# Kernel tuning notes

Hardware: AMD Instinct MI355X
Metric: run time of the kernel (lower is better)

Reference implementation:

```python
import jax, jax.numpy as jnp
import numpy as np

B, N, K, DIMS, F_DIMS = 2, 32768, 16, 2, 32
DS, DH, DO = 32, 32, 32
DA = DS + DH                      # 64
CH = (DIMS + 1) * (1 + K) + DIMS  # 53
CONV_IN = DIMS + (1 + K) * DA     # 1090
CONV_OUT = (1 + K) * DO           # 544


def setup_inputs() -> dict:
    key = jax.random.key(0)
    ks = jax.random.split(key, 6)
    s = 0.05
    return {
        "pc": jax.random.normal(ks[0], (B, N, 1 + K, DIMS), jnp.float32),
        "feats": jax.random.normal(ks[1], (B, N, 1 + K, F_DIMS), jnp.float32),
        "W_mlp": jax.random.normal(ks[2], (CH, DS), jnp.float32) * s,
        "b_mlp": jnp.zeros((DS,), jnp.float32),
        "W_att": jax.random.normal(ks[3], (DA, DA), jnp.float32) * s,
        "b_att": jnp.zeros((DA,), jnp.float32),
        "W_conv": jax.random.normal(ks[4], (CONV_IN, CONV_OUT), jnp.float32) * s,
        "b_conv": jnp.zeros((CONV_OUT,), jnp.float32),
        "W_skip": jax.random.normal(ks[5], (DO + F_DIMS, DO), jnp.float32) * s,
        "b_skip": jnp.zeros((DO,), jnp.float32),
    }


def reference(pc, feats, W_mlp, b_mlp, W_att, b_att, W_conv, b_conv, W_skip, b_skip):
    # ---- LocSE: relative-position encoding ----
    # rpbn_i[b,n,j] = concat(pc[b,n,i] - pc[b,n,j], ||pc[b,n,j]||)
    norms = jnp.linalg.norm(pc, axis=-1, keepdims=True)          # (B,N,1+K,1)
    # diffs[b,n,j,i,:] = pc[b,n,i,:] - pc[b,n,j,:]
    diffs = pc[:, :, None, :, :] - pc[:, :, :, None, :]          # (B,N,1+K,1+K,dims)
    norms_b = jnp.broadcast_to(norms[:, :, :, None, :], diffs.shape[:-1] + (1,))
    blocks = jnp.concatenate([diffs, norms_b], axis=-1)          # (B,N,1+K,1+K,dims+1)
    blocks = blocks.reshape(pc.shape[:3] + ((1 + K) * (DIMS + 1),))
    rppe = jnp.concatenate([pc, blocks], axis=-1)                # (B,N,1+K,CH)
    r = jax.nn.relu(rppe @ W_mlp + b_mlp)                        # (B,N,1+K,DS)
    se = jnp.concatenate([r, feats], axis=-1)                    # (B,N,1+K,DA)

    # ---- attention pooling (softmax over channel axis) ----
    att = jax.nn.softmax(se @ W_att + b_att, axis=-1) * se       # (B,N,1+K,DA)
    reshaped = att.reshape(att.shape[0], att.shape[1], (1 + K) * DA)

    cat = jnp.concatenate([pc[:, :, 0], reshaped], axis=-1)      # (B,N,CONV_IN)
    res = jax.nn.relu(cat @ W_conv + b_conv)                     # (B,N,(1+K)*DO)
    res = res.reshape(res.shape[0], res.shape[1], 1 + K, DO)

    skip_in = jnp.concatenate([feats, res], axis=-1)             # (B,N,1+K,F+DO)
    skip = jax.nn.relu(skip_in @ W_skip + b_skip)                # (B,N,1+K,DO)
    return skip
```

## Files before the change

### kernel.cpp

```cpp
#include <hip/hip_runtime.h>
#include <hip/hip_bf16.h>
#include <cstdint>

#define KNB      17
#define CH       53
#define MP       16
#define BM       64
#define NTHR     512
#define NRT      17
#define SE_LD    72
#define CATW     1120
#define RES_LD   552

#define NE_CONV  (35*34*512)
#define NE_MLP   (2*2*512)
#define NE_ATT   (2*4*512)
#define NE_SKIP  (2*2*512)
#define WS_MLP   (NE_CONV)
#define WS_ATT   (WS_MLP + NE_MLP)
#define WS_SKIP  (WS_ATT + NE_ATT)
#define WS_TOTAL (WS_SKIP + NE_SKIP)

typedef __bf16 bf16x8 __attribute__((ext_vector_type(8)));
typedef float  f32x4  __attribute__((ext_vector_type(4)));
typedef unsigned short u16x4 __attribute__((ext_vector_type(4)));
typedef unsigned short u16x8 __attribute__((ext_vector_type(8)));

__device__ __forceinline__ unsigned short f2b(float f) {
    union { __bf16 h; unsigned short u; } v; v.h = (__bf16)f; return v.u;
}
__device__ __forceinline__ float b2f(unsigned short b) {
    union { unsigned u; float f; } v; v.u = ((unsigned)b) << 16;
    return v.f;
}
__device__ __forceinline__ void gload_lds16(const void* g, void* l) {
    __builtin_amdgcn_global_load_lds(
        (const __attribute__((address_space(1))) unsigned int*)g,
        (__attribute__((address_space(3))) unsigned int*)l, 16, 0, 0);
}

__global__ void seac_prep(const float* __restrict__ Wmlp, const float* __restrict__ Watt,
                          const float* __restrict__ Wconv, const float* __restrict__ Wskip,
                          unsigned short* __restrict__ ws)
{
    int i = blockIdx.x * 256 + threadIdx.x;
    if (i >= WS_TOTAL) return;
    float v;
    if (i < WS_MLP) {
        int idx = i;
        int jj = idx & 7, l = (idx >> 3) & 63, t = idx >> 9;
        int nt = t % 34, ks = t / 34;
        int k = 32*ks + 8*(l >> 4) + jj;
        int o = 16*nt + (l & 15);
        int ok;
        if (k < 1088)       ok = k + 2;
        else if (k == 1088) ok = 0;
        else if (k == 1089) ok = 1;
        else                ok = -1;
        v = (ok >= 0) ? Wconv[ok*544 + o] : 0.f;
    } else if (i < WS_ATT) {
        int idx = i - WS_MLP;
        int jj = idx & 7, l = (idx >> 3) & 63, t = idx >> 9;
        int nt = t & 1, ks = t >> 1;
        int k = 32*ks + 8*(l >> 4) + jj;
        int o = 16*nt + (l & 15);
        v = (k < CH) ? Wmlp[k*32 + o] : 0.f;
    } else if (i < WS_SKIP) {
        int idx = i - WS_ATT;
        int jj = idx & 7, l = (idx >> 3) & 63, t = idx >> 9;
        int nt = t & 3, ks = t >> 2;
        int k = 32*ks + 8*(l >> 4) + jj;
        int o = 16*nt + (l & 15);
        v = Watt[k*64 + o];
    } else {
        int idx = i - WS_SKIP;
        int jj = idx & 7, l = (idx >> 3) & 63, t = idx >> 9;
        int nt = t & 1, ks = t >> 1;
        int k = 32*ks + 8*(l >> 4) + jj;
        int o = 16*nt + (l & 15);
        v = Wskip[k*32 + o];
    }
    ws[i] = f2b(v);
}

__global__ __launch_bounds__(NTHR, 6) void seac_locse(
    const float* __restrict__ pc, const float* __restrict__ feats,
    const float* __restrict__ bmlp, const float* __restrict__ batt,
    const unsigned short* __restrict__ ws, unsigned short* __restrict__ catg,
    int pt0)
{
    __shared__ unsigned short se_l[272 * SE_LD];
    __shared__ float pcl[MP][KNB][2];
    __shared__ float bmlp_l[32];
    __shared__ float batt_l[64];

    const int tid  = threadIdx.x;
    const int w    = tid >> 6;
    const int l    = tid & 63;
    const int g    = l >> 4;
    const int c15  = l & 15;
    const long pbase = (long)pt0 + (long)blockIdx.x * MP;
    const bf16x8* wsB8 = (const bf16x8*)ws;

    if (tid < MP*KNB) {
        int p = tid / KNB, i = tid - p*KNB;
        float x = pc[(pbase + p)*(KNB*2) + 2*i];
        float y = pc[(pbase + p)*(KNB*2) + 2*i + 1];
        pcl[p][i][0] = x; pcl[p][i][1] = y;
    }
    for (int q = tid; q < MP*544/4; q += NTHR) {
        float4 f = *(const float4*)&feats[pbase*544 + 4*q];
        int e0 = 4*q; int p = e0 / 544; int rem = e0 - 544*p;
        int j = rem >> 5, c = rem & 31;
        u16x4 u; u[0] = f2b(f.x); u[1] = f2b(f.y); u[2] = f2b(f.z); u[3] = f2b(f.w);
        *(u16x4*)&se_l[(p*KNB + j)*SE_LD + 32 + c] = u;
    }
    if (tid < 32)                     bmlp_l[tid]      = bmlp[tid];
    else if (tid >= 64 && tid < 128)  batt_l[tid-64]   = batt[tid-64];
    __syncthreads();

    {
        bf16x8 Bm[2][2];
        #pragma unroll
        for (int ks = 0; ks < 2; ++ks)
            #pragma unroll
            for (int nt = 0; nt < 2; ++nt)
                Bm[ks][nt] = wsB8[(WS_MLP >> 3) + (ks*2 + nt)*64 + l];
        float bch[2][4];
        #pragma unroll
        for (int nt = 0; nt < 2; ++nt)
            #pragma unroll
            for (int r = 0; r < 4; ++r) bch[nt][r] = bmlp_l[16*nt + 4*g + r];

        for (int mt = w; mt < NRT; mt += 8) {
            int row = 16*mt + c15;
            int p = row / KNB, j = row - p*KNB;
            float pjx = pcl[p][j][0], pjy = pcl[p][j][1];
            float nj = sqrtf(pjx*pjx + pjy*pjy);
            f32x4 acc0 = {0.f,0.f,0.f,0.f}, acc1 = {0.f,0.f,0.f,0.f};
            #pragma unroll
            for (int ks = 0; ks < 2; ++ks) {
                union { unsigned short u[8]; bf16x8 v; } a;
                #pragma unroll
                for (int jj = 0; jj < 8; ++jj) {
                    int k = 32*ks + 8*g + jj;
                    float vv;
                    if (k == 0) vv = pjx;
                    else if (k == 1) vv = pjy;
                    else if (k < CH) {
                        int kk = k - 2, ii = kk/3, t3 = kk - 3*ii;
                        vv = (t3 == 0) ? (pcl[p][ii][0] - pjx)
                           : (t3 == 1) ? (pcl[p][ii][1] - pjy) : nj;
                    } else vv = 0.f;
                    a.u[jj] = f2b(vv);
                }
                acc0 = __builtin_amdgcn_mfma_f32_16x16x32_bf16(Bm[ks][0], a.v, acc0, 0, 0, 0);
                acc1 = __builtin_amdgcn_mfma_f32_16x16x32_bf16(Bm[ks][1], a.v, acc1, 0, 0, 0);
            }
            u16x4 o0, o1;
            #pragma unroll
            for (int r = 0; r < 4; ++r) {
                o0[r] = f2b(fmaxf(acc0[r] + bch[0][r], 0.f));
                o1[r] = f2b(fmaxf(acc1[r] + bch[1][r], 0.f));
            }
            *(u16x4*)&se_l[row*SE_LD + 4*g]      = o0;
            *(u16x4*)&se_l[row*SE_LD + 16 + 4*g] = o1;
        }
    }
    __syncthreads();

    {
        bf16x8 Ba[2][4];
        #pragma unroll
        for (int ks = 0; ks < 2; ++ks)
            #pragma unroll
            for (int nt = 0; nt < 4; ++nt)
                Ba[ks][nt] = wsB8[(WS_ATT >> 3) + (ks*4 + nt)*64 + l];
        float bch[16];
        #pragma unroll
        for (int nt = 0; nt < 4; ++nt)
            #pragma unroll
            for (int r = 0; r < 4; ++r) bch[4*nt+r] = batt_l[16*nt + 4*g + r];

        for (int mt = w; mt < NRT; mt += 8) {
            int row = 16*mt + c15;
            bf16x8 b0 = *(const bf16x8*)&se_l[row*SE_LD + 8*g];
            bf16x8 b1 = *(const bf16x8*)&se_l[row*SE_LD + 32 + 8*g];
            f32x4 acc[4];
            #pragma unroll
            for (int nt = 0; nt < 4; ++nt) {
                f32x4 z = {0.f,0.f,0.f,0.f};
                acc[nt] = __builtin_amdgcn_mfma_f32_16x16x32_bf16(Ba[0][nt], b0, z,       0, 0, 0);
                acc[nt] = __builtin_amdgcn_mfma_f32_16x16x32_bf16(Ba[1][nt], b1, acc[nt], 0, 0, 0);
            }
            float vv[16];
            #pragma unroll
            for (int nt = 0; nt < 4; ++nt)
                #pragma unroll
                for (int r = 0; r < 4; ++r) vv[4*nt+r] = acc[nt][r] + bch[4*nt+r];
            float m = vv[0];
            #pragma unroll
            for (int i = 1; i < 16; ++i) m = fmaxf(m, vv[i]);
            m = fmaxf(m, __shfl_xor(m, 16)); m = fmaxf(m, __shfl_xor(m, 32));
            float s = 0.f;
            #pragma unroll
            for (int i = 0; i < 16; ++i) { vv[i] = __expf(vv[i] - m); s += vv[i]; }
            s += __shfl_xor(s, 16); s += __shfl_xor(s, 32);
            float inv = 1.f / s;
            #pragma unroll
            for (int nt = 0; nt < 4; ++nt) {
                u16x4 sv = *(const u16x4*)&se_l[row*SE_LD + 16*nt + 4*g];
                u16x4 ov;
                #pragma unroll
                for (int r = 0; r < 4; ++r) ov[r] = f2b(vv[4*nt+r]*inv * b2f(sv[r]));
                *(u16x4*)&se_l[row*SE_LD + 16*nt + 4*g] = ov;
            }
        }
    }
    __syncthreads();

    for (int c = tid; c < MP*140; c += NTHR) {
        int p = c / 140, rem = c - 140*p;
        int e = 8*rem;
        u16x8 v;
        if (e < 1088) {
            int row = p*KNB + (e >> 6), col = e & 63;
            v = *(const u16x8*)&se_l[row*SE_LD + col];
        } else {
            #pragma unroll
            for (int q = 0; q < 8; ++q) v[q] = 0;
            if (e == 1088) { v[0] = f2b(pcl[p][0][0]); v[1] = f2b(pcl[p][0][1]); }
        }
        *(u16x8*)&catg[(pbase + p)*CATW + e] = v;
    }
}

__global__ __launch_bounds__(NTHR, 4) void seac_conv(
    const unsigned short* __restrict__ catg, const float* __restrict__ feats,
    const float* __restrict__ bconv, const float* __restrict__ bskip,
    const unsigned short* __restrict__ ws, float* __restrict__ out, int pt0)
{
    __shared__ unsigned short astage[4][BM][32];
    __shared__ unsigned short res_l[32 * RES_LD];
    __shared__ float bconv_l[544];

    const int tid  = threadIdx.x;
    const int w    = tid >> 6;
    const int l    = tid & 63;
    const int g    = l >> 4;
    const int c15  = l & 15;
    const long pbase = (long)pt0 + (long)blockIdx.x * BM;
    const bf16x8* wsB8 = (const bf16x8*)ws;

    for (int i = tid; i < 544; i += NTHR) bconv_l[i] = bconv[i];

    if (tid < 256) {
        const unsigned short* g0 = &catg[(pbase + (tid >> 2))*CATW + 8*(tid & 3)];
        gload_lds16(g0,      &astage[0][16*(tid >> 6)][0]);
        gload_lds16(g0 + 32, &astage[1][16*(tid >> 6)][0]);
        gload_lds16(g0 + 64, &astage[2][16*(tid >> 6)][0]);
    }

    f32x4 acc[4][5];
    #pragma unroll
    for (int mt = 0; mt < 4; ++mt)
        #pragma unroll
        for (int t = 0; t < 5; ++t) { f32x4 z = {0.f,0.f,0.f,0.f}; acc[mt][t] = z; }

    for (int ks = 0; ks < 35; ++ks) {
        asm volatile("s_waitcnt vmcnt(2)" ::: "memory");
        __builtin_amdgcn_s_barrier();
        __builtin_amdgcn_sched_barrier(0);
        bf16x8 a[4];
        #pragma unroll
        for (int mt = 0; mt < 4; ++mt)
            a[mt] = *(const bf16x8*)&astage[ks & 3][16*mt + c15][8*g];
        #pragma unroll
        for (int t = 0; t < 5; ++t) {
            int nt = w + 8*t;
            if (nt < 34) {
                bf16x8 b = wsB8[(ks*34 + nt)*64 + l];
                #pragma unroll
                for (int mt = 0; mt < 4; ++mt)
                    acc[mt][t] = __builtin_amdgcn_mfma_f32_16x16x32_bf16(a[mt], b, acc[mt][t], 0, 0, 0);
            }
        }
        if (ks + 3 < 35 && tid < 256)
            gload_lds16(&catg[(pbase + (tid >> 2))*CATW + 32*(ks+3) + 8*(tid & 3)],
                        &astage[(ks+3) & 3][16*(tid >> 6)][0]);
    }
    __syncthreads();

    bf16x8 Bs[2][2];
    #pragma unroll
    for (int ks = 0; ks < 2; ++ks)
        #pragma unroll
        for (int nt = 0; nt < 2; ++nt)
            Bs[ks][nt] = wsB8[(WS_SKIP >> 3) + (ks*2 + nt)*64 + l];
    float bs0 = bskip[c15], bs1 = bskip[16 + c15];

    #pragma unroll
    for (int half = 0; half < 2; ++half) {
        #pragma unroll
        for (int t = 0; t < 5; ++t) {
            int nt = w + 8*t;
            if (nt < 34) {
                float bc = bconv_l[16*nt + c15];
                #pragma unroll
                for (int mh = 0; mh < 2; ++mh) {
                    int mt = 2*half + mh;
                    #pragma unroll
                    for (int r = 0; r < 4; ++r)
                        res_l[(16*mh + 4*g + r)*RES_LD + 16*nt + c15] =
                            f2b(fmaxf(acc[mt][t][r] + bc, 0.f));
                }
            }
        }
        __syncthreads();

        const long gofs = pbase*KNB + 544*half;
        for (int tt = 0; tt < 5; ++tt) {
            int mt2 = w + 8*tt;
            if (mt2 < 34) {
                int rr = 16*mt2 + c15;
                int pp = rr / 17, jn = rr - 17*pp;
                float4 f0 = *(const float4*)&feats[(gofs + rr)*32 + 8*g];
                float4 f1 = *(const float4*)&feats[(gofs + rr)*32 + 8*g + 4];
                union { unsigned short u[8]; bf16x8 v; } af;
                af.u[0]=f2b(f0.x); af.u[1]=f2b(f0.y); af.u[2]=f2b(f0.z); af.u[3]=f2b(f0.w);
                af.u[4]=f2b(f1.x); af.u[5]=f2b(f1.y); af.u[6]=f2b(f1.z); af.u[7]=f2b(f1.w);
                bf16x8 ar = *(const bf16x8*)&res_l[pp*RES_LD + 32*jn + 8*g];
                f32x4 z = {0.f,0.f,0.f,0.f};
                f32x4 a0 = __builtin_amdgcn_mfma_f32_16x16x32_bf16(af.v, Bs[0][0], z, 0, 0, 0);
                a0       = __builtin_amdgcn_mfma_f32_16x16x32_bf16(ar,   Bs[1][0], a0, 0, 0, 0);
                f32x4 a1 = __builtin_amdgcn_mfma_f32_16x16x32_bf16(af.v, Bs[0][1], z, 0, 0, 0);
                a1       = __builtin_amdgcn_mfma_f32_16x16x32_bf16(ar,   Bs[1][1], a1, 0, 0, 0);
                #pragma unroll
                for (int r = 0; r < 4; ++r) {
                    long orow = gofs + 16*mt2 + 4*g + r;
                    out[orow*32 + c15]      = fmaxf(a0[r] + bs0, 0.f);
                    out[orow*32 + 16 + c15] = fmaxf(a1[r] + bs1, 0.f);
                }
            }
        }
        if (half == 0) __syncthreads();
    }
}

extern "C" void kernel_launch(void* const* d_in, const int* in_sizes, int n_in,
                              void* d_out, int out_size, void* d_ws, size_t ws_size,
                              hipStream_t stream)
{
    const float* pc    = (const float*)d_in[0];
    const float* feats = (const float*)d_in[1];
    const float* Wmlp  = (const float*)d_in[2];
    const float* bmlp  = (const float*)d_in[3];
    const float* Watt  = (const float*)d_in[4];
    const float* batt  = (const float*)d_in[5];
    const float* Wconv = (const float*)d_in[6];
    const float* bconv = (const float*)d_in[7];
    const float* Wskip = (const float*)d_in[8];
    const float* bskip = (const float*)d_in[9];
    float* out = (float*)d_out;
    unsigned short* ws16 = (unsigned short*)d_ws;

    int npts = in_sizes[0] / (KNB*2);

    size_t frag_bytes = (size_t)WS_TOTAL * 2;
    size_t cat_off    = (frag_bytes + 255) & ~(size_t)255;
    unsigned short* catg = (unsigned short*)((char*)d_ws + cat_off);
    size_t avail = (ws_size > cat_off) ? (ws_size - cat_off) : 0;
    long maxpts = (long)(avail / (CATW * 2));
    long chunk  = (maxpts / BM) * BM;
    if (chunk > npts) chunk = npts;
    if (chunk < BM)   chunk = BM;

    int prep_blocks = (WS_TOTAL + 255) / 256;
    hipLaunchKernelGGL(seac_prep, dim3(prep_blocks), dim3(256), 0, stream,
                       Wmlp, Watt, Wconv, Wskip, ws16);

    for (long base = 0; base < npts; base += chunk) {
        long c = npts - base; if (c > chunk) c = chunk;
        hipLaunchKernelGGL(seac_locse, dim3((int)(c / MP)), dim3(NTHR), 0, stream,
                           pc, feats, bmlp, batt, ws16, catg, (int)base);
        hipLaunchKernelGGL(seac_conv, dim3((int)(c / BM)), dim3(NTHR), 0, stream,
                           catg, feats, bconv, bskip, ws16, out, (int)base);
    }
}
```

Baseline: 316.6 us.

## Double-buffer conv A-tiles in five-step super-stages to cut barriers

The conv GEMM's A-operand staging changes from a 4-deep ring with one barrier and waitcnt per 32-wide K step to double-buffered super-stages of five K steps. All 8 waves now issue the global-to-LDS loads, and there is one __syncthreads per super-stage. The aim is to cut per-step barrier overhead and spread the staging loads over more waves. The risks are fewer K steps of lookahead at the start of each super-stage, a larger LDS footprint (two buffers of 5×64×32 bf16), and possibly lower occupancy.

```diff
diff --git a/kernel.cpp b/kernel.cpp
--- a/kernel.cpp
+++ b/kernel.cpp
@@ -11,6 +11,8 @@
 #define SE_LD    72
 #define CATW     1120
 #define RES_LD   552
+#define KSPAN    5
+#define NSUPER   7
 
 #define NE_CONV  (35*34*512)
 #define NE_MLP   (2*2*512)
@@ -240,7 +242,7 @@
     const float* __restrict__ bconv, const float* __restrict__ bskip,
     const unsigned short* __restrict__ ws, float* __restrict__ out, int pt0)
 {
-    __shared__ unsigned short astage[4][BM][32];
+    __shared__ unsigned short astage[2][KSPAN][BM][32];
     __shared__ unsigned short res_l[32 * RES_LD];
     __shared__ float bconv_l[544];
 
@@ -254,12 +256,22 @@
 
     for (int i = tid; i < 544; i += NTHR) bconv_l[i] = bconv[i];
 
-    if (tid < 256) {
-        const unsigned short* g0 = &catg[(pbase + (tid >> 2))*CATW + 8*(tid & 3)];
-        gload_lds16(g0,      &astage[0][16*(tid >> 6)][0]);
-        gload_lds16(g0 + 32, &astage[1][16*(tid >> 6)][0]);
-        gload_lds16(g0 + 64, &astage[2][16*(tid >> 6)][0]);
-    }
+    #define STAGE(s, b)                                                            \
+        _Pragma("unroll")                                                          \
+        for (int r = 0; r < 3; ++r) {                                              \
+            int q0 = 64*(8*r + w);                                                 \
+            if (q0 < KSPAN*256) {                                                  \
+                int q   = q0 + l;                                                  \
+                int ksl = q >> 8;                                                  \
+                int p   = (q >> 2) & 63;                                           \
+                int gr  = q & 3;                                                   \
+                gload_lds16(&catg[(pbase + p)*CATW + 32*(KSPAN*(s) + ksl) + 8*gr], \
+                            &astage[b][0][0][0] + (size_t)q0*8);                   \
+            }                                                                      \
+        }
+
+    STAGE(0, 0);
+    __syncthreads();
 
     f32x4 acc[4][5];
     #pragma unroll
@@ -267,29 +279,31 @@
         #pragma unroll
         for (int t = 0; t < 5; ++t) { f32x4 z = {0.f,0.f,0.f,0.f}; acc[mt][t] = z; }
 
-    for (int ks = 0; ks < 35; ++ks) {
-        asm volatile("s_waitcnt vmcnt(2)" ::: "memory");
-        __builtin_amdgcn_s_barrier();
-        __builtin_amdgcn_sched_barrier(0);
-        bf16x8 a[4];
-        #pragma unroll
-        for (int mt = 0; mt < 4; ++mt)
-            a[mt] = *(const bf16x8*)&astage[ks & 3][16*mt + c15][8*g];
-        #pragma unroll
-        for (int t = 0; t < 5; ++t) {
-            int nt = w + 8*t;
-            if (nt < 34) {
-                bf16x8 b = wsB8[(ks*34 + nt)*64 + l];
-                #pragma unroll
-                for (int mt = 0; mt < 4; ++mt)
-                    acc[mt][t] = __builtin_amdgcn_mfma_f32_16x16x32_bf16(a[mt], b, acc[mt][t], 0, 0, 0);
-            }
-        }
-        if (ks + 3 < 35 && tid < 256)
-            gload_lds16(&catg[(pbase + (tid >> 2))*CATW + 32*(ks+3) + 8*(tid & 3)],
-                        &astage[(ks+3) & 3][16*(tid >> 6)][0]);
-    }
-    __syncthreads();
+    int buf = 0;
+    for (int s = 0; s < NSUPER; ++s) {
+        if (s + 1 < NSUPER) { STAGE(s+1, buf^1); }
+        #pragma unroll
+        for (int ksl = 0; ksl < KSPAN; ++ksl) {
+            int ks = KSPAN*s + ksl;
+            bf16x8 a[4];
+            #pragma unroll
+            for (int mt = 0; mt < 4; ++mt)
+                a[mt] = *(const bf16x8*)&astage[buf][ksl][16*mt + c15][8*g];
+            #pragma unroll
+            for (int t = 0; t < 5; ++t) {
+                int nt = w + 8*t;
+                if (nt < 34) {
+                    bf16x8 b = wsB8[(ks*34 + nt)*64 + l];
+                    #pragma unroll
+                    for (int mt = 0; mt < 4; ++mt)
+                        acc[mt][t] = __builtin_amdgcn_mfma_f32_16x16x32_bf16(a[mt], b, acc[mt][t], 0, 0, 0);
+                }
+            }
+        }
+        __syncthreads();
+        buf ^= 1;
+    }
+    #undef STAGE
 
     bf16x8 Bs[2][2];
     #pragma unroll
```

New measurement: 414.3 us. 30.9% more time.
